# Kernel optimization log

Hardware: AMD Instinct MI355X
Metric: run time of the kernel (lower is better)

## Reference

```python
import jax, jax.numpy as jnp
import numpy as np

NL, D, Di, N, R, K, V, NH = 24, 768, 1536, 16, 48, 4, 50280, 12
BATCH, SEQ = 4, 256


def setup_inputs():
    key = jax.random.key(0)
    it = iter(jax.random.split(key, 48))
    g = lambda shape, s=0.02: jax.random.normal(next(it), shape, jnp.float32) * s
    inp = {
        "question_ids": jax.random.randint(next(it), (BATCH, SEQ), 0, V),
        "question_mask": jnp.ones((BATCH, SEQ), jnp.int32),
        "answer_ids": jax.random.randint(next(it), (BATCH, SEQ), 0, V),
        "answer_mask": jnp.ones((BATCH, SEQ), jnp.int32),
        "embed": g((V, D)),
        "norm_w": jnp.ones((NL, D)),
        "in_proj_w": g((NL, 2 * Di, D)),
        "conv_w": g((NL, Di, K), 0.1),
        "conv_b": jnp.zeros((NL, Di)),
        "x_proj_w": g((NL, R + 2 * N, Di)),
        "dt_proj_w": g((NL, Di, R)),
        "dt_proj_b": g((NL, Di), 0.5) - 4.0,
        "A_log": jnp.log(jnp.broadcast_to(jnp.arange(1, N + 1, dtype=jnp.float32), (NL, Di, N))) + 0.0,
        "D_p": jnp.ones((NL, Di)),
        "out_proj_w": g((NL, D, Di)),
        "norm_f": jnp.ones((D,)),
        "ln1_w": jnp.ones((D,)), "ln1_b": jnp.zeros((D,)),
        "qkv_w": g((3 * D, D)), "qkv_b": jnp.zeros((3 * D,)),
        "attn_out_w": g((D, D)), "attn_out_b": jnp.zeros((D,)),
        "ln2_w": jnp.ones((D,)), "ln2_b": jnp.zeros((D,)),
        "ff1_w": g((4 * D, D)), "ff1_b": jnp.zeros((4 * D,)),
        "ff2_w": g((D, 4 * D)), "ff2_b": jnp.zeros((D,)),
        "C_w": g((1, N)), "proj_out_w": g((D, Di)),
        "B_w": g((N, 1)), "proj_in_w": g((Di, D), 0.002),
    }
    return inp


def _rms(x, w, eps=1e-5):
    return x * jax.lax.rsqrt(jnp.mean(x * x, axis=-1, keepdims=True) + eps) * w


def _ln(x, w, b, eps=1e-5):
    m = jnp.mean(x, axis=-1, keepdims=True)
    v = jnp.var(x, axis=-1, keepdims=True)
    return (x - m) * jax.lax.rsqrt(v + eps) * w + b


def _mamba_block(h, layer, init_state):
    nw, ipw, cw, cb, xpw, dpw, dpb, alog, dp, opw = layer
    x_in = _rms(h, nw)
    xz = jnp.einsum('bld,ed->ble', x_in, ipw)  # (B,L,2*Di)
    x, z = jnp.split(xz, 2, axis=-1)
    L = x.shape[1]
    xp = jnp.pad(x, ((0, 0), (K - 1, 0), (0, 0)))  # causal depthwise conv, kernel K
    x = sum(xp[:, k:k + L, :] * cw[:, k] for k in range(K)) + cb
    x = jax.nn.silu(x)
    dbl = jnp.einsum('bld,ed->ble', x, xpw)
    dt, Bm, Cm = dbl[..., :R], dbl[..., R:R + N], dbl[..., R + N:]
    delta = jax.nn.softplus(jnp.einsum('blr,dr->bld', dt, dpw) + dpb)  # (B,L,Di)
    A = -jnp.exp(alog)  # (Di,N)

    def step(hs, t):  # selective scan, carry (B,Di,N)
        d_t, x_t, B_t, C_t = t
        hs = jnp.exp(d_t[..., None] * A) * hs + (d_t * x_t)[..., None] * B_t[:, None, :]
        return hs, jnp.einsum('bdn,bn->bd', hs, C_t)

    xs = tuple(jnp.moveaxis(a, 1, 0) for a in (delta, x, Bm, Cm))
    last, ys = jax.lax.scan(step, init_state, xs)
    y = jnp.moveaxis(ys, 0, 1) + x * dp
    y = y * jax.nn.silu(z)
    return h + jnp.einsum('bld,od->blo', y, opw), last


def _backbone(ids, mask, embed, mamba_params, norm_f, init_states):
    h = embed[ids] * mask[..., None].astype(embed.dtype)
    block = jax.checkpoint(_mamba_block)  # remat per layer: bounds bwd memory

    def layer_step(carry, xs):
        *layer, st = xs
        return block(carry, tuple(layer), st)

    h, lasts = jax.lax.scan(layer_step, h, mamba_params + (init_states,))
    h = _rms(h, norm_f)
    return jnp.einsum('bld,vd->blv', h, embed), lasts  # tied lm head


def _tf_layer(x, ln1_w, ln1_b, qkv_w, qkv_b, attn_out_w, attn_out_b, ln2_w, ln2_b, ff1_w, ff1_b, ff2_w, ff2_b):
    B, S, _ = x.shape
    hd = D // NH
    y = _ln(x, ln1_w, ln1_b)  # norm_first pre-LN
    q, k, v = jnp.split(y @ qkv_w.T + qkv_b, 3, axis=-1)
    q = q.reshape(B, S, NH, hd); k = k.reshape(B, S, NH, hd); v = v.reshape(B, S, NH, hd)
    att = jax.nn.softmax(jnp.einsum('bqhd,bkhd->bhqk', q, k) / jnp.sqrt(jnp.float32(hd)), axis=-1)
    o = jnp.einsum('bhqk,bkhd->bqhd', att, v).reshape(B, S, D)
    x = x + o @ attn_out_w.T + attn_out_b
    y = _ln(x, ln2_w, ln2_b)
    return x + jax.nn.gelu(y @ ff1_w.T + ff1_b, approximate=False) @ ff2_w.T + ff2_b


def _refine(states, C_w, proj_out_w, B_w, proj_in_w, tf_params):
    # states: (B, NL, Di, N); 12-step recurrent state refinement
    for _ in range(12):
        d = jnp.einsum('bsdn,n->bsd', states, C_w[0])  # C: Linear(16,1), squeeze(-1)
        d = jnp.einsum('bsd,od->bso', d, proj_out_w)   # 1536 -> 768
        d = _tf_layer(d, *tf_params)
        d = jnp.einsum('bso,do->bsd', d, proj_in_w)    # 768 -> 1536
        states = states + d[..., None] * B_w[:, 0]     # B: Linear(1,16)
    return states


def reference(question_ids, question_mask, answer_ids, answer_mask, embed, norm_w, in_proj_w, conv_w, conv_b, x_proj_w, dt_proj_w, dt_proj_b, A_log, D_p, out_proj_w, norm_f, ln1_w, ln1_b, qkv_w, qkv_b, attn_out_w, attn_out_b, ln2_w, ln2_b, ff1_w, ff1_b, ff2_w, ff2_b, C_w, proj_out_w, B_w, proj_in_w):
    mamba_params = (norm_w, in_proj_w, conv_w, conv_b, x_proj_w, dt_proj_w, dt_proj_b, A_log, D_p, out_proj_w)
    tf_params = (ln1_w, ln1_b, qkv_w, qkv_b, attn_out_w, attn_out_b, ln2_w, ln2_b, ff1_w, ff1_b, ff2_w, ff2_b)
    Bsz = question_ids.shape[0]
    zeros = jnp.zeros((NL, Bsz, Di, N), embed.dtype)
    _, lasts = _backbone(question_ids, question_mask, embed, mamba_params, norm_f, zeros)
    states = jnp.moveaxis(lasts, 0, 1)  # torch.stack(states, dim=1): (B, NL, Di, N)
    states = _refine(states, C_w, proj_out_w, B_w, proj_in_w, tf_params)
    logits, _ = _backbone(answer_ids, answer_mask, embed, mamba_params, norm_f, jnp.moveaxis(states, 0, 1))
    return logits
```

## Files before the change

### kernel.cpp

```cpp
#include <hip/hip_runtime.h>
#include <math.h>

namespace {

constexpr int kNL = 24, kD = 768, kDi = 1536, kN = 16, kR = 48, kK = 4, kV = 50280, kNH = 12;
constexpr int kB = 4, kS = 256;
constexpr int kMtok = kB * kS;
constexpr int kMref = kB * kNL;
constexpr int kVp = 50304;

using bf16x8   = __attribute__((ext_vector_type(8))) short;
using f32x4    = __attribute__((ext_vector_type(4))) float;
using ushort8v = __attribute__((ext_vector_type(8))) unsigned short;

__device__ __forceinline__ float siluf(float x) { return x / (1.f + __expf(-x)); }

__device__ __forceinline__ ushort f2b(float f) {
    union { float f; unsigned u; } v; v.f = f;
    unsigned u = v.u;
    unsigned r = (u + 0x7FFFu + ((u >> 16) & 1u)) >> 16;
    return (ushort)r;
}
__device__ __forceinline__ float b2f(ushort u) {
    union { unsigned u; float f; } v; v.u = (unsigned)u << 16; return v.f;
}

#define GLOAD_LDS(g, l) \
    __builtin_amdgcn_global_load_lds((const __attribute__((address_space(1))) void*)(g), \
                                     (__attribute__((address_space(3))) void*)(l), 16, 0, 0)

template <int BM, int BN, int BIAS, int ACT, int RES, int OUTMODE, int PIPE, int SSQ = 0>
__global__ __launch_bounds__(256, (PIPE == 3 ? 3 : 2)) void gemm_bf16(
    const ushort* __restrict__ A, int lda,
    const ushort* __restrict__ B, int ldb,
    float* __restrict__ C, int ldc,
    ushort* __restrict__ Cbf, int ldcb,
    float* __restrict__ C2,
    const float* __restrict__ bias,
    const float* __restrict__ aux,
    int M, int N, int K)
{
    constexpr int ACH = BM / 32;
    constexpr int BCH = BN / 32;
    constexpr int MI  = BM / 32;
    constexpr int NJ  = BN / 32;

    __shared__ ushort As[PIPE][BM * 64];
    __shared__ ushort Bs[PIPE][BN * 64];

    const int tid  = threadIdx.x;
    const int lane = tid & 63;
    const int wave = tid >> 6;
    const int m0 = blockIdx.y * BM;
    const int n0 = blockIdx.x * BN;
    const int wr = (wave >> 1) * (BM / 2);
    const int wc = (wave & 1) * (BN / 2);

    f32x4 acc[MI][NJ];
#pragma unroll
    for (int i = 0; i < MI; ++i)
#pragma unroll
        for (int j = 0; j < NJ; ++j) acc[i][j] = f32x4{0.f, 0.f, 0.f, 0.f};

    const int srow = lane >> 3;
    const int scol = ((lane & 7) ^ srow) * 8;
    const ushort* gA[ACH];
    const ushort* gB[BCH];
#pragma unroll
    for (int g = 0; g < ACH; ++g)
        gA[g] = A + (size_t)(m0 + (g * 4 + wave) * 8 + srow) * lda + scol;
#pragma unroll
    for (int g = 0; g < BCH; ++g)
        gB[g] = B + (size_t)(n0 + (g * 4 + wave) * 8 + srow) * ldb + scol;

    const int frow = lane & 15;
    const int kh   = lane >> 4;
    const int nt   = K >> 6;

    auto stage = [&](int t, int buf) {
        const int off = t * 64;
#pragma unroll
        for (int g = 0; g < ACH; ++g) GLOAD_LDS(gA[g] + off, &As[buf][(g * 4 + wave) * 512]);
#pragma unroll
        for (int g = 0; g < BCH; ++g) GLOAD_LDS(gB[g] + off, &Bs[buf][(g * 4 + wave) * 512]);
    };
    auto compute = [&](int buf) {
#pragma unroll
        for (int s = 0; s < 2; ++s) {
            bf16x8 fa[MI], fb[NJ];
#pragma unroll
            for (int i = 0; i < MI; ++i) {
                int r = wr + i * 16 + frow;
                int slot = (s * 4 + kh) ^ (r & 7);
                fa[i] = *(const bf16x8*)&As[buf][r * 64 + slot * 8];
            }
#pragma unroll
            for (int j = 0; j < NJ; ++j) {
                int r = wc + j * 16 + frow;
                int slot = (s * 4 + kh) ^ (r & 7);
                fb[j] = *(const bf16x8*)&Bs[buf][r * 64 + slot * 8];
            }
#pragma unroll
            for (int i = 0; i < MI; ++i)
#pragma unroll
                for (int j = 0; j < NJ; ++j)
                    acc[i][j] = __builtin_amdgcn_mfma_f32_16x16x32_bf16(fa[i], fb[j], acc[i][j], 0, 0, 0);
        }
    };

    if constexpr (PIPE == 3) {
        stage(0, 0);
        if (nt > 1) stage(1, 1);
        for (int t = 0; t < nt; ++t) {
            if (t < nt - 1) {
                asm volatile("s_waitcnt vmcnt(%0)" :: "n"(ACH + BCH) : "memory");
            } else {
                asm volatile("s_waitcnt vmcnt(0)" ::: "memory");
            }
            __builtin_amdgcn_s_barrier();
            if (t + 2 < nt) stage(t + 2, (t + 2) % 3);
            compute(t % 3);
        }
        __builtin_amdgcn_s_barrier();
    } else {
        stage(0, 0);
        __syncthreads();
        int cur = 0;
        for (int t = 0; t < nt; ++t) {
            if (t + 1 < nt) stage(t + 1, cur ^ 1);
            compute(cur);
            __syncthreads();
            cur ^= 1;
        }
    }

    const int ccol = lane & 15;
    const int crow = (lane >> 4) * 4;
    float rsq[MI][4];
    if constexpr (SSQ) {
#pragma unroll
        for (int i = 0; i < MI; ++i)
#pragma unroll
            for (int q = 0; q < 4; ++q) rsq[i][q] = 0.f;
    }
#pragma unroll
    for (int i = 0; i < MI; ++i) {
#pragma unroll
        for (int j = 0; j < NJ; ++j) {
            int gn = n0 + wc + j * 16 + ccol;
            if (gn >= N) continue;
            float bv = BIAS ? bias[gn] : 0.f;
#pragma unroll
            for (int q = 0; q < 4; ++q) {
                int gm = m0 + wr + i * 16 + crow + q;
                if (gm >= M) continue;
                float v = acc[i][j][q] + bv;
                if (ACT == 1) v = fmaxf(v, 0.f) + log1pf(expf(-fabsf(v)));
                if (ACT == 2) v = 0.5f * v * (1.f + erff(v * 0.70710678118654752f));
                if (OUTMODE == 3) {
                    if (gn < 48) Cbf[(size_t)gm * 64 + gn] = f2b(v);
                    else if (gn < 64) { Cbf[(size_t)gm * 64 + gn] = 0; C2[(size_t)(gn - 48) * kMtok + gm] = v; }
                    else if (gn < 80) C2[(size_t)(gn - 48) * kMtok + gm] = v;
                } else if (OUTMODE == 4) {
                    ((ushort*)C2)[(size_t)gn * kMtok + gm] = f2b(v);
                } else if (OUTMODE == 7) {
                    int bb = gm / kNL, ss = gm - bb * kNL;
                    float* stp = C2 + ((size_t)(ss * kB + bb) * kDi + gn) * kN;
                    float a2 = 0.f;
#pragma unroll
                    for (int nn = 0; nn < kN; ++nn) {
                        float sv = stp[nn] + v * bias[nn];
                        stp[nn] = sv;
                        a2 += sv * aux[nn];
                    }
                    Cbf[(size_t)gm * ldcb + gn] = f2b(a2);
                } else {
                    size_t ci = (size_t)gm * ldc + gn;
                    if (RES) v += C[ci];
                    if (OUTMODE != 2) C[ci] = v;
                    if (OUTMODE == 1 || OUTMODE == 2) Cbf[(size_t)gm * ldcb + gn] = f2b(v);
                    if constexpr (SSQ) rsq[i][q] += v * v;
                }
            }
        }
    }
    if constexpr (SSQ) {
#pragma unroll
        for (int i = 0; i < MI; ++i)
#pragma unroll
            for (int q = 0; q < 4; ++q) {
                rsq[i][q] += __shfl_xor(rsq[i][q], 1, 16);
                rsq[i][q] += __shfl_xor(rsq[i][q], 2, 16);
                rsq[i][q] += __shfl_xor(rsq[i][q], 4, 16);
                rsq[i][q] += __shfl_xor(rsq[i][q], 8, 16);
            }
        float* red = (float*)&As[0][0];
        __syncthreads();
        if ((lane & 15) == 0) {
#pragma unroll
            for (int i = 0; i < MI; ++i)
#pragma unroll
                for (int q = 0; q < 4; ++q) {
                    int rl = (wave >> 1) * 32 + i * 16 + (lane >> 4) * 4 + q;
                    red[(wave & 1) * 64 + rl] = rsq[i][q];
                }
        }
        __syncthreads();
        if (tid < 64) C2[(size_t)blockIdx.x * kMtok + m0 + tid] = red[tid] + red[64 + tid];
    }
}

template <int BM, int BN, int BIAS, int ACT, int RES, int OUTMODE, int PIPE, int SSQ = 0>
static void gemm(const ushort* A, int lda, const ushort* B, int ldb,
                 float* C, int ldc, ushort* Cb, int ldcb, float* C2,
                 const float* bias, const float* aux, int M, int N, int K, hipStream_t s)
{
    dim3 g((N + BN - 1) / BN, (M + BM - 1) / BM);
    gemm_bf16<BM, BN, BIAS, ACT, RES, OUTMODE, PIPE, SSQ><<<g, dim3(256), 0, s>>>(
        A, lda, B, ldb, C, ldc, Cb, ldcb, C2, bias, aux, M, N, K);
}

__global__ __launch_bounds__(256, 4) void gemm_rms(
    const float* __restrict__ hbuf, const float* __restrict__ ssq,
    const float* __restrict__ nw,
    const ushort* __restrict__ B, int ldb,
    ushort* __restrict__ Xbf, ushort* __restrict__ zTb,
    int M, int N, int K)
{
    constexpr int MI = 2, NJ = 2, BCH = 2;
    __shared__ ushort As[2][64 * 64];
    __shared__ ushort Bs[2][64 * 64];
    const int tid  = threadIdx.x;
    const int lane = tid & 63;
    const int wave = tid >> 6;
    const int m0 = blockIdx.y * 64;
    const int n0 = blockIdx.x * 64;
    const int wr = (wave >> 1) * 32;
    const int wc = (wave & 1) * 32;

    f32x4 acc[MI][NJ];
#pragma unroll
    for (int i = 0; i < MI; ++i)
#pragma unroll
        for (int j = 0; j < NJ; ++j) acc[i][j] = f32x4{0.f, 0.f, 0.f, 0.f};

    const int srow = lane >> 3;
    const int scol = ((lane & 7) ^ srow) * 8;
    const ushort* gB[BCH];
#pragma unroll
    for (int g = 0; g < BCH; ++g)
        gB[g] = B + (size_t)(n0 + (g * 4 + wave) * 8 + srow) * ldb + scol;

    int arow[2];
    float rs[2];
#pragma unroll
    for (int g = 0; g < 2; ++g) {
        arow[g] = m0 + (g * 4 + wave) * 8 + srow;
        float s = 0.f;
#pragma unroll
        for (int c = 0; c < 12; ++c) s += ssq[c * kMtok + arow[g]];
        rs[g] = rsqrtf(s * (1.f / 768.f) + 1e-5f);
    }

    const int frow = lane & 15;
    const int kh   = lane >> 4;
    const int nt   = K >> 6;

    float4 av[2][2], wv[2];
    auto loadA = [&](int t) {
        int k = t * 64 + scol;
        wv[0] = *(const float4*)&nw[k];
        wv[1] = *(const float4*)&nw[k + 4];
#pragma unroll
        for (int g = 0; g < 2; ++g) {
            av[g][0] = *(const float4*)&hbuf[(size_t)arow[g] * K + k];
            av[g][1] = *(const float4*)&hbuf[(size_t)arow[g] * K + k + 4];
        }
    };
    auto writeA = [&](int buf) {
#pragma unroll
        for (int g = 0; g < 2; ++g) {
            ushort8v o;
            o[0] = f2b(av[g][0].x * rs[g] * wv[0].x);
            o[1] = f2b(av[g][0].y * rs[g] * wv[0].y);
            o[2] = f2b(av[g][0].z * rs[g] * wv[0].z);
            o[3] = f2b(av[g][0].w * rs[g] * wv[0].w);
            o[4] = f2b(av[g][1].x * rs[g] * wv[1].x);
            o[5] = f2b(av[g][1].y * rs[g] * wv[1].y);
            o[6] = f2b(av[g][1].z * rs[g] * wv[1].z);
            o[7] = f2b(av[g][1].w * rs[g] * wv[1].w);
            *(ushort8v*)&As[buf][(g * 4 + wave) * 512 + lane * 8] = o;
        }
    };
    auto stageB = [&](int t, int buf) {
#pragma unroll
        for (int g = 0; g < BCH; ++g) GLOAD_LDS(gB[g] + t * 64, &Bs[buf][(g * 4 + wave) * 512]);
    };
    auto compute = [&](int buf) {
#pragma unroll
        for (int s = 0; s < 2; ++s) {
            bf16x8 fa[MI], fb[NJ];
#pragma unroll
            for (int i = 0; i < MI; ++i) {
                int r = wr + i * 16 + frow;
                int slot = (s * 4 + kh) ^ (r & 7);
                fa[i] = *(const bf16x8*)&As[buf][r * 64 + slot * 8];
            }
#pragma unroll
            for (int j = 0; j < NJ; ++j) {
                int r = wc + j * 16 + frow;
                int slot = (s * 4 + kh) ^ (r & 7);
                fb[j] = *(const bf16x8*)&Bs[buf][r * 64 + slot * 8];
            }
#pragma unroll
            for (int i = 0; i < MI; ++i)
#pragma unroll
                for (int j = 0; j < NJ; ++j)
                    acc[i][j] = __builtin_amdgcn_mfma_f32_16x16x32_bf16(fa[i], fb[j], acc[i][j], 0, 0, 0);
        }
    };

    loadA(0);
    stageB(0, 0);
    writeA(0);
    __syncthreads();
    int cur = 0;
    for (int t = 0; t < nt; ++t) {
        if (t + 1 < nt) { loadA(t + 1); stageB(t + 1, cur ^ 1); }
        compute(cur);
        if (t + 1 < nt) writeA(cur ^ 1);
        __syncthreads();
        cur ^= 1;
    }

    const int ccol = lane & 15;
    const int crow = (lane >> 4) * 4;
#pragma unroll
    for (int i = 0; i < MI; ++i) {
#pragma unroll
        for (int j = 0; j < NJ; ++j) {
            int gn = n0 + wc + j * 16 + ccol;
#pragma unroll
            for (int q = 0; q < 4; ++q) {
                int gm = m0 + wr + i * 16 + crow + q;
                float v = acc[i][j][q];
                if (gn < kDi) Xbf[(size_t)gm * kDi + gn] = f2b(v);
                else zTb[(size_t)(gn - kDi) * kMtok + gm] = f2b(siluf(v));
            }
        }
    }
}

__global__ void cvt_kernel(const float* __restrict__ src, ushort* __restrict__ dst, int n) {
    int i = (blockIdx.x * 256 + threadIdx.x) * 4;
    if (i >= n) return;
    float4 v = *(const float4*)(src + i);
    ushort4 o; o.x = f2b(v.x); o.y = f2b(v.y); o.z = f2b(v.z); o.w = f2b(v.w);
    *(ushort4*)(dst + i) = o;
}

__global__ void cvt_xpw_kernel(const float* __restrict__ src, ushort* __restrict__ dst) {
    int i = (blockIdx.x * 256 + threadIdx.x) * 4;
    if (i >= 24 * 80 * 1536) return;
    int l = i / (80 * 1536), r = i - l * (80 * 1536);
    int row = r / 1536, col = r - row * 1536;
    float4 v = *(const float4*)(src + i);
    ushort4 o; o.x = f2b(v.x); o.y = f2b(v.y); o.z = f2b(v.z); o.w = f2b(v.w);
    *(ushort4*)(dst + ((size_t)(l * 128 + row)) * 1536 + col) = o;
}

__global__ void cvt_dpw_kernel(const float* __restrict__ src, ushort* __restrict__ dst) {
    int i = blockIdx.x * 256 + threadIdx.x;
    if (i >= 24 * 1536 * 64) return;
    int col = i & 63, row = i >> 6;
    dst[i] = (col < 48) ? f2b(src[(size_t)row * 48 + col]) : (ushort)0;
}

__global__ void embed_kernel(const int* __restrict__ ids, const int* __restrict__ msk,
                             const float* __restrict__ embed, float* __restrict__ h,
                             float* __restrict__ ssq)
{
    int i = blockIdx.x * 256 + threadIdx.x;
    int row = i / kD, col = i - row * kD;
    float v = embed[(size_t)ids[row] * kD + col] * (float)msk[row];
    h[i] = v;
    float s = v * v;
    s += __shfl_xor(s, 1);  s += __shfl_xor(s, 2);  s += __shfl_xor(s, 4);
    s += __shfl_xor(s, 8);  s += __shfl_xor(s, 16); s += __shfl_xor(s, 32);
    if ((threadIdx.x & 63) == 0) ssq[(col >> 6) * kMtok + row] = s;
}

__global__ __launch_bounds__(256) void rms_kernel(const float* __restrict__ x,
                                                  const float* __restrict__ w,
                                                  ushort* __restrict__ out)
{
    __shared__ float red[256];
    int row = blockIdx.x, tid = threadIdx.x;
    const float* xr = x + (size_t)row * kD;
    float s = 0.f;
    for (int j = tid; j < kD; j += 256) { float v = xr[j]; s += v * v; }
    red[tid] = s; __syncthreads();
    for (int o = 128; o > 0; o >>= 1) { if (tid < o) red[tid] += red[tid + o]; __syncthreads(); }
    float rs = rsqrtf(red[0] / (float)kD + 1e-5f);
    for (int j = tid; j < kD; j += 256) out[(size_t)row * kD + j] = f2b(xr[j] * rs * w[j]);
}

__global__ __launch_bounds__(256) void ln_kernel(const float* __restrict__ x,
                                                 const float* __restrict__ w,
                                                 const float* __restrict__ b,
                                                 ushort* __restrict__ out)
{
    __shared__ float r1[256], r2[256];
    int row = blockIdx.x, tid = threadIdx.x;
    const float* xr = x + (size_t)row * kD;
    float s = 0.f, s2 = 0.f;
    for (int j = tid; j < kD; j += 256) { float v = xr[j]; s += v; s2 += v * v; }
    r1[tid] = s; r2[tid] = s2; __syncthreads();
    for (int o = 128; o > 0; o >>= 1) {
        if (tid < o) { r1[tid] += r1[tid + o]; r2[tid] += r2[tid + o]; }
        __syncthreads();
    }
    float mean = r1[0] / (float)kD;
    float var = r2[0] / (float)kD - mean * mean;
    float rsv = rsqrtf(var + 1e-5f);
    for (int j = tid; j < kD; j += 256)
        out[(size_t)row * kD + j] = f2b((xr[j] - mean) * rsv * w[j] + b[j]);
}

__global__ __launch_bounds__(256) void conv_kernel(
    const ushort* __restrict__ xb, const float* __restrict__ cw,
    const float* __restrict__ cb, ushort* __restrict__ xc_bf,
    ushort* __restrict__ xcT)
{
    int d   = blockIdx.x * 256 + threadIdx.x;
    int bt0 = blockIdx.y * 16;
    int t0  = bt0 & (kS - 1);
    float w0 = cw[d * 4], w1 = cw[d * 4 + 1], w2 = cw[d * 4 + 2], w3 = cw[d * 4 + 3];
    float bias = cb[d];
    float xv[19];
#pragma unroll
    for (int j = 0; j < 19; ++j) {
        int tt = t0 - 3 + j;
        xv[j] = (tt >= 0) ? b2f(xb[(size_t)(bt0 - 3 + j) * kDi + d]) : 0.f;
    }
    ushort8v o0, o1;
#pragma unroll
    for (int e = 0; e < 16; ++e) {
        float s = bias + xv[e] * w0 + xv[e + 1] * w1 + xv[e + 2] * w2 + xv[e + 3] * w3;
        ushort us = f2b(siluf(s));
        xc_bf[(size_t)(bt0 + e) * kDi + d] = us;
        if (e < 8) o0[e] = us; else o1[e - 8] = us;
    }
    *(ushort8v*)(xcT + (size_t)d * kMtok + bt0)     = o0;
    *(ushort8v*)(xcT + (size_t)d * kMtok + bt0 + 8) = o1;
}

__global__ __launch_bounds__(256) void scan_kernel(
    const ushort* __restrict__ dltT, const ushort* __restrict__ xcT,
    const ushort* __restrict__ zT, const float* __restrict__ bcT,
    const float* __restrict__ alog, const float* __restrict__ dp,
    float* __restrict__ states, ushort* __restrict__ y)
{
    int gid = blockIdx.x * 256 + threadIdx.x;
    int n = gid & 15;
    int d = (gid >> 4) % kDi;
    int b = gid / (kDi * kN);
    float Areg = -__expf(alog[d * kN + n]);
    float dpv = dp[d];
    size_t sidx = (size_t)(b * kDi + d) * kN + n;
    float hs = states[sidx];
    const ushort8v* pD = (const ushort8v*)(dltT + (size_t)d * kMtok + b * kS);
    const ushort8v* pX = (const ushort8v*)(xcT  + (size_t)d * kMtok + b * kS);
    const ushort8v* pZ = (const ushort8v*)(zT   + (size_t)d * kMtok + b * kS);
    const float4* pB = (const float4*)(bcT + (size_t)n * kMtok + b * kS);
    const float4* pC = (const float4*)(bcT + (size_t)(16 + n) * kMtok + b * kS);
    ushort8v D = pD[0], X = pX[0], Z = pZ[0];
    float4 B0 = pB[0], B1 = pB[1], C0 = pC[0], C1 = pC[1];
    ushort* yrow = y + (size_t)(b * kS) * kDi + d;
    for (int g = 0; g < kS / 8; ++g) {
        ushort8v Dn, Xn, Zn; float4 Bn0, Bn1, Cn0, Cn1;
        if (g + 1 < kS / 8) {
            Dn = pD[g + 1]; Xn = pX[g + 1]; Zn = pZ[g + 1];
            Bn0 = pB[2 * g + 2]; Bn1 = pB[2 * g + 3];
            Cn0 = pC[2 * g + 2]; Cn1 = pC[2 * g + 3];
        }
#pragma unroll
        for (int e = 0; e < 8; ++e) {
            float dv = b2f(D[e]), xv = b2f(X[e]), zv = b2f(Z[e]);
            float Bv = (e < 4) ? (&B0.x)[e] : (&B1.x)[e - 4];
            float Cv = (e < 4) ? (&C0.x)[e] : (&C1.x)[e - 4];
            hs = __expf(dv * Areg) * hs + (dv * xv) * Bv;
            float p = hs * Cv;
            p += __shfl_xor(p, 1, 16);
            p += __shfl_xor(p, 2, 16);
            p += __shfl_xor(p, 4, 16);
            p += __shfl_xor(p, 8, 16);
            if (n == 0) yrow[(size_t)(g * 8 + e) * kDi] = f2b((p + xv * dpv) * zv);
        }
        D = Dn; X = Xn; Z = Zn; B0 = Bn0; B1 = Bn1; C0 = Cn0; C1 = Cn1;
    }
    states[sidx] = hs;
}

__global__ void contract_kernel(const float* __restrict__ st, const float* __restrict__ Cw,
                                ushort* __restrict__ dDi)
{
    int i = blockIdx.x * 256 + threadIdx.x;
    int row = i / kDi, di = i - row * kDi;
    int b = row / kNL, s = row - b * kNL;
    const float* sp = st + ((size_t)(s * kB + b) * kDi + di) * kN;
    float acc = 0.f;
#pragma unroll
    for (int nn = 0; nn < kN; ++nn) acc += sp[nn] * Cw[nn];
    dDi[i] = f2b(acc);
}

__global__ __launch_bounds__(32) void attn_kernel(const float* __restrict__ qkv,
                                                  ushort* __restrict__ o)
{
    int b = blockIdx.x / kNH;
    int hh = blockIdx.x - b * kNH;
    int sq = threadIdx.x;
    if (sq >= kNL) return;
    const float* qrow = qkv + (size_t)(b * kNL + sq) * (3 * kD) + hh * 64;
    float q[64];
#pragma unroll
    for (int e = 0; e < 64; ++e) q[e] = qrow[e];
    float sc[kNL];
    float mx = -1e30f;
    for (int sk = 0; sk < kNL; ++sk) {
        const float* krow = qkv + (size_t)(b * kNL + sk) * (3 * kD) + kD + hh * 64;
        float dt = 0.f;
#pragma unroll
        for (int e = 0; e < 64; ++e) dt += q[e] * krow[e];
        dt *= 0.125f;
        sc[sk] = dt;
        mx = fmaxf(mx, dt);
    }
    float sum = 0.f;
    for (int sk = 0; sk < kNL; ++sk) { sc[sk] = expf(sc[sk] - mx); sum += sc[sk]; }
    float inv = 1.f / sum;
    float out[64];
#pragma unroll
    for (int e = 0; e < 64; ++e) out[e] = 0.f;
    for (int sk = 0; sk < kNL; ++sk) {
        float wgt = sc[sk] * inv;
        const float* vrow = qkv + (size_t)(b * kNL + sk) * (3 * kD) + 2 * kD + hh * 64;
#pragma unroll
        for (int e = 0; e < 64; ++e) out[e] += wgt * vrow[e];
    }
    ushort* orow = o + (size_t)(b * kNL + sq) * kD + hh * 64;
#pragma unroll
    for (int e = 0; e < 64; ++e) orow[e] = f2b(out[e]);
}

}

extern "C" void kernel_launch(void* const* d_in, const int* in_sizes, int n_in,
                              void* d_out, int out_size, void* d_ws, size_t ws_size,
                              hipStream_t stream)
{
    const int*   q_ids  = (const int*)d_in[0];
    const int*   q_msk  = (const int*)d_in[1];
    const int*   a_ids  = (const int*)d_in[2];
    const int*   a_msk  = (const int*)d_in[3];
    const float* embed  = (const float*)d_in[4];
    const float* norm_w = (const float*)d_in[5];
    const float* ipw    = (const float*)d_in[6];
    const float* cw     = (const float*)d_in[7];
    const float* cb     = (const float*)d_in[8];
    const float* xpw    = (const float*)d_in[9];
    const float* dpw    = (const float*)d_in[10];
    const float* dpb    = (const float*)d_in[11];
    const float* alog   = (const float*)d_in[12];
    const float* dpp    = (const float*)d_in[13];
    const float* opw    = (const float*)d_in[14];
    const float* norm_f = (const float*)d_in[15];
    const float* ln1w   = (const float*)d_in[16];
    const float* ln1b   = (const float*)d_in[17];
    const float* qkvw   = (const float*)d_in[18];
    const float* qkvbi  = (const float*)d_in[19];
    const float* aow    = (const float*)d_in[20];
    const float* aob    = (const float*)d_in[21];
    const float* ln2w   = (const float*)d_in[22];
    const float* ln2b   = (const float*)d_in[23];
    const float* ff1w   = (const float*)d_in[24];
    const float* ff1b   = (const float*)d_in[25];
    const float* ff2w   = (const float*)d_in[26];
    const float* ff2b   = (const float*)d_in[27];
    const float* Cwp    = (const float*)d_in[28];
    const float* powp   = (const float*)d_in[29];
    const float* Bwp    = (const float*)d_in[30];
    const float* piwp   = (const float*)d_in[31];

    char* base = (char*)d_ws;
    size_t cur = 0;
    auto allocB = [&](size_t bytes) { char* p = base + cur; cur = (cur + bytes + 255) & ~(size_t)255; return p; };
    auto allocF = [&](size_t n) { return (float*)allocB(n * 4); };
    auto allocH = [&](size_t n) { return (ushort*)allocB(n * 2); };

    float* h     = allocF((size_t)kMtok * kD);
    float* ssqp  = allocF((size_t)12 * kMtok);
    float* bcT   = allocF((size_t)32 * kMtok);
    float* st    = allocF((size_t)kNL * kB * kDi * kN);
    float* x768  = allocF((size_t)kMref * kD);
    float* qkvB  = allocF((size_t)kMref * 3 * kD);
    ushort* x_bf    = allocH((size_t)kMtok * kDi);
    ushort* zT_b    = allocH((size_t)kDi * kMtok);
    ushort* xcT_b   = allocH((size_t)kDi * kMtok);
    ushort* dltT_b  = allocH((size_t)kDi * kMtok);
    ushort* xc_bf   = allocH((size_t)kMtok * kDi);
    ushort* dtin_bf = allocH((size_t)kMtok * 64);
    ushort* yb_bf   = allocH((size_t)kMtok * kDi);
    ushort* xin_bf  = allocH((size_t)kMtok * kD);
    ushort* dDi_bf  = allocH((size_t)128 * kDi);
    ushort* tb_bf   = allocH((size_t)128 * kD);
    ushort* o768_bf = allocH((size_t)128 * kD);
    ushort* f3_bf   = allocH((size_t)128 * 4 * kD);
    ushort* x768_bf = allocH((size_t)128 * kD);
    ushort* xpw_bf  = allocH((size_t)kNL * 128 * kDi);
    ushort* dpw_bf  = allocH((size_t)kNL * kDi * 64);
    ushort* powp_bf = allocH((size_t)kD * kDi);
    ushort* qkvw_bf = allocH((size_t)3 * kD * kD);
    ushort* aow_bf  = allocH((size_t)kD * kD);
    ushort* ff1w_bf = allocH((size_t)4 * kD * kD);
    ushort* ff2w_bf = allocH((size_t)kD * 4 * kD);
    ushort* piw_bf  = allocH((size_t)kDi * kD);
    ushort* emb_bf  = allocH((size_t)kVp * kD);

    size_t base_end = cur;
    ushort* ipw_all = allocH((size_t)kNL * 2 * kDi * kD);
    ushort* opw_all = allocH((size_t)kNL * kD * kDi);
    bool full = (cur <= ws_size);
    ushort* ipw_stg = nullptr;
    ushort* opw_stg = nullptr;
    if (!full) {
        cur = base_end;
        ipw_stg = allocH((size_t)2 * kDi * kD);
        opw_stg = allocH((size_t)kD * kDi);
        if (cur > ws_size) return;
    }

    auto cvt = [&](const float* s, ushort* d, size_t n) {
        cvt_kernel<<<dim3((unsigned)((n / 4 + 255) / 256)), dim3(256), 0, stream>>>(s, d, (int)n);
    };

    hipMemsetAsync(st, 0, sizeof(float) * (size_t)kNL * kB * kDi * kN, stream);

    cvt_xpw_kernel<<<dim3(2880), dim3(256), 0, stream>>>(xpw, xpw_bf);
    cvt_dpw_kernel<<<dim3(9216), dim3(256), 0, stream>>>(dpw, dpw_bf);
    cvt(powp, powp_bf, (size_t)kD * kDi);
    cvt(qkvw, qkvw_bf, (size_t)3 * kD * kD);
    cvt(aow,  aow_bf,  (size_t)kD * kD);
    cvt(ff1w, ff1w_bf, (size_t)4 * kD * kD);
    cvt(ff2w, ff2w_bf, (size_t)kD * 4 * kD);
    cvt(piwp, piw_bf,  (size_t)kDi * kD);
    cvt(embed, emb_bf, (size_t)kV * kD);
    if (full) {
        cvt(ipw, ipw_all, (size_t)kNL * 2 * kDi * kD);
        cvt(opw, opw_all, (size_t)kNL * kD * kDi);
    }

    for (int pass = 0; pass < 2; ++pass) {
        const int* ids = pass ? a_ids : q_ids;
        const int* msk = pass ? a_msk : q_msk;

        embed_kernel<<<dim3(kMtok * kD / 256), dim3(256), 0, stream>>>(ids, msk, embed, h, ssqp);

        for (int l = 0; l < kNL; ++l) {
            const ushort* ipw_l;
            const ushort* opw_l;
            if (full) {
                ipw_l = ipw_all + (size_t)l * 2 * kDi * kD;
                opw_l = opw_all + (size_t)l * kD * kDi;
            } else {
                cvt(ipw + (size_t)l * 2 * kDi * kD, ipw_stg, (size_t)2 * kDi * kD);
                cvt(opw + (size_t)l * kD * kDi, opw_stg, (size_t)kD * kDi);
                ipw_l = ipw_stg;
                opw_l = opw_stg;
            }
            gemm_rms<<<dim3(48, 16), dim3(256), 0, stream>>>(
                h, ssqp, norm_w + (size_t)l * kD, ipw_l, kD, x_bf, zT_b, kMtok, 2 * kDi, kD);
            conv_kernel<<<dim3(kDi / 256, kMtok / 16), dim3(256), 0, stream>>>(
                x_bf, cw + (size_t)l * kDi * kK, cb + (size_t)l * kDi, xc_bf, xcT_b);
            gemm<64, 64, 0, 0, 0, 3, 3>(xc_bf, kDi, xpw_bf + (size_t)l * 128 * kDi, kDi,
                                        nullptr, 0, dtin_bf, 0, bcT,
                                        nullptr, nullptr, kMtok, 128, kDi, stream);
            gemm<64, 64, 1, 1, 0, 4, 3>(dtin_bf, 64, dpw_bf + (size_t)l * kDi * 64, 64,
                                        nullptr, 0, nullptr, 0, (float*)dltT_b,
                                        dpb + (size_t)l * kDi, nullptr, kMtok, kDi, 64, stream);
            scan_kernel<<<dim3(kB * kDi * kN / 256), dim3(256), 0, stream>>>(
                dltT_b, xcT_b, zT_b, bcT, alog + (size_t)l * kDi * kN, dpp + (size_t)l * kDi,
                st + (size_t)l * kB * kDi * kN, yb_bf);
            gemm<64, 64, 0, 0, 1, 0, 3, 1>(yb_bf, kDi, opw_l, kDi, h, kD, nullptr, 0, ssqp,
                                           nullptr, nullptr, kMtok, kD, kDi, stream);
        }

        if (pass == 0) {
            contract_kernel<<<dim3(kMref * kDi / 256), dim3(256), 0, stream>>>(st, Cwp, dDi_bf);
            for (int it = 0; it < 12; ++it) {
                gemm<64, 64, 0, 0, 0, 0, 3>(dDi_bf, kDi, powp_bf, kDi, x768, kD, nullptr, 0, nullptr,
                                            nullptr, nullptr, kMref, kD, kDi, stream);
                ln_kernel<<<dim3(kMref), dim3(256), 0, stream>>>(x768, ln1w, ln1b, tb_bf);
                gemm<64, 64, 1, 0, 0, 0, 3>(tb_bf, kD, qkvw_bf, kD, qkvB, 3 * kD, nullptr, 0, nullptr,
                                            qkvbi, nullptr, kMref, 3 * kD, kD, stream);
                attn_kernel<<<dim3(kB * kNH), dim3(32), 0, stream>>>(qkvB, o768_bf);
                gemm<64, 64, 1, 0, 1, 0, 3>(o768_bf, kD, aow_bf, kD, x768, kD, nullptr, 0, nullptr,
                                            aob, nullptr, kMref, kD, kD, stream);
                ln_kernel<<<dim3(kMref), dim3(256), 0, stream>>>(x768, ln2w, ln2b, tb_bf);
                gemm<64, 64, 1, 2, 0, 2, 3>(tb_bf, kD, ff1w_bf, kD, nullptr, 0, f3_bf, 4 * kD, nullptr,
                                            ff1b, nullptr, kMref, 4 * kD, kD, stream);
                gemm<64, 64, 1, 0, 1, 1, 3>(f3_bf, 4 * kD, ff2w_bf, 4 * kD, x768, kD, x768_bf, kD, nullptr,
                                            ff2b, nullptr, kMref, kD, 4 * kD, stream);
                gemm<64, 64, 0, 0, 0, 7, 3>(x768_bf, kD, piw_bf, kD, nullptr, 0, dDi_bf, kDi, st,
                                            Bwp, Cwp, kMref, kDi, kD, stream);
            }
        } else {
            rms_kernel<<<dim3(kMtok), dim3(256), 0, stream>>>(h, norm_f, xin_bf);
            gemm<128, 128, 0, 0, 0, 0, 2>(xin_bf, kD, emb_bf, kD, (float*)d_out, kV, nullptr, 0, nullptr,
                                          nullptr, nullptr, kMtok, kV, kD, stream);
        }
    }
}
```

Measured before the change: 8.637 ms.

## Fuse LayerNorm into GEMMs and fold ff2 with proj_in in refine loop

Removes the two standalone LayerNorm kernels in the refine loop. The preceding GEMMs now emit per-row partial sum and sum-of-squares, and a new gemm_ln kernel normalizes the A operand on the fly while staging it. It also precomputes proj_in·ff2 as one combined weight with a folded bias, so the ff2 GEMM and the proj_in GEMM become a single GEMM over a concatenated K=3840 operand [x | gelu(ff1)]. This cuts kernel launches and intermediate traffic in the 12-iteration refine loop, at the cost of extra setup GEMMs and different bf16 rounding from the reassociated products.

```diff
diff --git a/kernel.cpp b/kernel.cpp
--- a/kernel.cpp
+++ b/kernel.cpp
@@ -8,6 +8,7 @@
 constexpr int kMtok = kB * kS;
 constexpr int kMref = kB * kNL;
 constexpr int kVp = 50304;
+constexpr int kKa = 3840;
 
 using bf16x8   = __attribute__((ext_vector_type(8))) short;
 using f32x4    = __attribute__((ext_vector_type(4))) float;
@@ -38,6 +39,7 @@
     float* __restrict__ C2,
     const float* __restrict__ bias,
     const float* __restrict__ aux,
+    const float* __restrict__ aux2,
     int M, int N, int K)
 {
     constexpr int ACH = BM / 32;
@@ -136,12 +138,12 @@
 
     const int ccol = lane & 15;
     const int crow = (lane >> 4) * 4;
-    float rsq[MI][4];
+    float rsq[MI][4], rsm[MI][4];
     if constexpr (SSQ) {
 #pragma unroll
         for (int i = 0; i < MI; ++i)
 #pragma unroll
-            for (int q = 0; q < 4; ++q) rsq[i][q] = 0.f;
+            for (int q = 0; q < 4; ++q) { rsq[i][q] = 0.f; rsm[i][q] = 0.f; }
     }
 #pragma unroll
     for (int i = 0; i < MI; ++i) {
@@ -169,7 +171,7 @@
                     float a2 = 0.f;
 #pragma unroll
                     for (int nn = 0; nn < kN; ++nn) {
-                        float sv = stp[nn] + v * bias[nn];
+                        float sv = stp[nn] + v * aux2[nn];
                         stp[nn] = sv;
                         a2 += sv * aux[nn];
                     }
@@ -179,7 +181,7 @@
                     if (RES) v += C[ci];
                     if (OUTMODE != 2) C[ci] = v;
                     if (OUTMODE == 1 || OUTMODE == 2) Cbf[(size_t)gm * ldcb + gn] = f2b(v);
-                    if constexpr (SSQ) rsq[i][q] += v * v;
+                    if constexpr (SSQ) { rsq[i][q] += v * v; rsm[i][q] += v; }
                 }
             }
         }
@@ -193,6 +195,12 @@
                 rsq[i][q] += __shfl_xor(rsq[i][q], 2, 16);
                 rsq[i][q] += __shfl_xor(rsq[i][q], 4, 16);
                 rsq[i][q] += __shfl_xor(rsq[i][q], 8, 16);
+                if (SSQ == 2) {
+                    rsm[i][q] += __shfl_xor(rsm[i][q], 1, 16);
+                    rsm[i][q] += __shfl_xor(rsm[i][q], 2, 16);
+                    rsm[i][q] += __shfl_xor(rsm[i][q], 4, 16);
+                    rsm[i][q] += __shfl_xor(rsm[i][q], 8, 16);
+                }
             }
         float* red = (float*)&As[0][0];
         __syncthreads();
@@ -201,23 +209,33 @@
             for (int i = 0; i < MI; ++i)
 #pragma unroll
                 for (int q = 0; q < 4; ++q) {
-                    int rl = (wave >> 1) * 32 + i * 16 + (lane >> 4) * 4 + q;
-                    red[(wave & 1) * 64 + rl] = rsq[i][q];
+                    int rl = (wave >> 1) * (BM / 2) + i * 16 + (lane >> 4) * 4 + q;
+                    red[(wave & 1) * BM + rl] = rsq[i][q];
+                    if (SSQ == 2) red[2 * BM + (wave & 1) * BM + rl] = rsm[i][q];
                 }
         }
         __syncthreads();
-        if (tid < 64) C2[(size_t)blockIdx.x * kMtok + m0 + tid] = red[tid] + red[64 + tid];
+        if (tid < BM) {
+            if (SSQ == 1) {
+                C2[(size_t)blockIdx.x * kMtok + m0 + tid] = red[tid] + red[BM + tid];
+            } else {
+                C2[(size_t)blockIdx.x * 128 + m0 + tid] = red[tid] + red[BM + tid];
+                C2[(size_t)gridDim.x * 128 + blockIdx.x * 128 + m0 + tid] =
+                    red[2 * BM + tid] + red[3 * BM + tid];
+            }
+        }
     }
 }
 
 template <int BM, int BN, int BIAS, int ACT, int RES, int OUTMODE, int PIPE, int SSQ = 0>
 static void gemm(const ushort* A, int lda, const ushort* B, int ldb,
                  float* C, int ldc, ushort* Cb, int ldcb, float* C2,
-                 const float* bias, const float* aux, int M, int N, int K, hipStream_t s)
+                 const float* bias, const float* aux, int M, int N, int K, hipStream_t s,
+                 const float* aux2 = nullptr)
 {
     dim3 g((N + BN - 1) / BN, (M + BM - 1) / BM);
     gemm_bf16<BM, BN, BIAS, ACT, RES, OUTMODE, PIPE, SSQ><<<g, dim3(256), 0, s>>>(
-        A, lda, B, ldb, C, ldc, Cb, ldcb, C2, bias, aux, M, N, K);
+        A, lda, B, ldb, C, ldc, Cb, ldcb, C2, bias, aux, aux2, M, N, K);
 }
 
 __global__ __launch_bounds__(256, 4) void gemm_rms(
@@ -351,6 +369,151 @@
     }
 }
 
+template <int ACT, int OUTBF>
+__global__ __launch_bounds__(256, 4) void gemm_ln(
+    const float* __restrict__ hbuf, const float* __restrict__ pp,
+    const float* __restrict__ lw, const float* __restrict__ lb,
+    const ushort* __restrict__ B, int ldb,
+    float* __restrict__ C, int ldc,
+    ushort* __restrict__ Cbf, int ldcb,
+    const float* __restrict__ bias,
+    int M, int N, int K)
+{
+    constexpr int MI = 2, NJ = 2, BCH = 2, NP = 12;
+    __shared__ ushort As[2][64 * 64];
+    __shared__ ushort Bs[2][64 * 64];
+    const int tid  = threadIdx.x;
+    const int lane = tid & 63;
+    const int wave = tid >> 6;
+    const int m0 = blockIdx.y * 64;
+    const int n0 = blockIdx.x * 64;
+    const int wr = (wave >> 1) * 32;
+    const int wc = (wave & 1) * 32;
+
+    f32x4 acc[MI][NJ];
+#pragma unroll
+    for (int i = 0; i < MI; ++i)
+#pragma unroll
+        for (int j = 0; j < NJ; ++j) acc[i][j] = f32x4{0.f, 0.f, 0.f, 0.f};
+
+    const int srow = lane >> 3;
+    const int scol = ((lane & 7) ^ srow) * 8;
+    const ushort* gB[BCH];
+#pragma unroll
+    for (int g = 0; g < BCH; ++g)
+        gB[g] = B + (size_t)(n0 + (g * 4 + wave) * 8 + srow) * ldb + scol;
+
+    int arow[2];
+    float mean[2], rsv[2];
+#pragma unroll
+    for (int g = 0; g < 2; ++g) {
+        arow[g] = m0 + (g * 4 + wave) * 8 + srow;
+        float sq = 0.f, sm = 0.f;
+#pragma unroll
+        for (int c = 0; c < NP; ++c) {
+            sq += pp[c * 128 + arow[g]];
+            sm += pp[NP * 128 + c * 128 + arow[g]];
+        }
+        float mu = sm * (1.f / 768.f);
+        mean[g] = mu;
+        rsv[g] = rsqrtf(sq * (1.f / 768.f) - mu * mu + 1e-5f);
+    }
+
+    const int frow = lane & 15;
+    const int kh   = lane >> 4;
+    const int nt   = K >> 6;
+
+    float4 av[2][2], wv[2], bv2[2];
+    auto loadA = [&](int t) {
+        int k = t * 64 + scol;
+        wv[0]  = *(const float4*)&lw[k];
+        wv[1]  = *(const float4*)&lw[k + 4];
+        bv2[0] = *(const float4*)&lb[k];
+        bv2[1] = *(const float4*)&lb[k + 4];
+#pragma unroll
+        for (int g = 0; g < 2; ++g) {
+            av[g][0] = *(const float4*)&hbuf[(size_t)arow[g] * K + k];
+            av[g][1] = *(const float4*)&hbuf[(size_t)arow[g] * K + k + 4];
+        }
+    };
+    auto writeA = [&](int buf) {
+#pragma unroll
+        for (int g = 0; g < 2; ++g) {
+            ushort8v o;
+            o[0] = f2b((av[g][0].x - mean[g]) * rsv[g] * wv[0].x + bv2[0].x);
+            o[1] = f2b((av[g][0].y - mean[g]) * rsv[g] * wv[0].y + bv2[0].y);
+            o[2] = f2b((av[g][0].z - mean[g]) * rsv[g] * wv[0].z + bv2[0].z);
+            o[3] = f2b((av[g][0].w - mean[g]) * rsv[g] * wv[0].w + bv2[0].w);
+            o[4] = f2b((av[g][1].x - mean[g]) * rsv[g] * wv[1].x + bv2[1].x);
+            o[5] = f2b((av[g][1].y - mean[g]) * rsv[g] * wv[1].y + bv2[1].y);
+            o[6] = f2b((av[g][1].z - mean[g]) * rsv[g] * wv[1].z + bv2[1].z);
+            o[7] = f2b((av[g][1].w - mean[g]) * rsv[g] * wv[1].w + bv2[1].w);
+            *(ushort8v*)&As[buf][(g * 4 + wave) * 512 + lane * 8] = o;
+        }
+    };
+    auto stageB = [&](int t, int buf) {
+#pragma unroll
+        for (int g = 0; g < BCH; ++g) GLOAD_LDS(gB[g] + t * 64, &Bs[buf][(g * 4 + wave) * 512]);
+    };
+    auto compute = [&](int buf) {
+#pragma unroll
+        for (int s = 0; s < 2; ++s) {
+            bf16x8 fa[MI], fb[NJ];
+#pragma unroll
+            for (int i = 0; i < MI; ++i) {
+                int r = wr + i * 16 + frow;
+                int slot = (s * 4 + kh) ^ (r & 7);
+                fa[i] = *(const bf16x8*)&As[buf][r * 64 + slot * 8];
+            }
+#pragma unroll
+            for (int j = 0; j < NJ; ++j) {
+                int r = wc + j * 16 + frow;
+                int slot = (s * 4 + kh) ^ (r & 7);
+                fb[j] = *(const bf16x8*)&Bs[buf][r * 64 + slot * 8];
+            }
+#pragma unroll
+            for (int i = 0; i < MI; ++i)
+#pragma unroll
+                for (int j = 0; j < NJ; ++j)
+                    acc[i][j] = __builtin_amdgcn_mfma_f32_16x16x32_bf16(fa[i], fb[j], acc[i][j], 0, 0, 0);
+        }
+    };
+
+    loadA(0);
+    stageB(0, 0);
+    writeA(0);
+    __syncthreads();
+    int cur = 0;
+    for (int t = 0; t < nt; ++t) {
+        if (t + 1 < nt) { loadA(t + 1); stageB(t + 1, cur ^ 1); }
+        compute(cur);
+        if (t + 1 < nt) writeA(cur ^ 1);
+        __syncthreads();
+        cur ^= 1;
+    }
+
+    const int ccol = lane & 15;
+    const int crow = (lane >> 4) * 4;
+#pragma unroll
+    for (int i = 0; i < MI; ++i) {
+#pragma unroll
+        for (int j = 0; j < NJ; ++j) {
+            int gn = n0 + wc + j * 16 + ccol;
+            if (gn >= N) continue;
+            float bvv = bias[gn];
+#pragma unroll
+            for (int q = 0; q < 4; ++q) {
+                int gm = m0 + wr + i * 16 + crow + q;
+                if (gm >= M) continue;
+                float v = acc[i][j][q] + bvv;
+                if (ACT == 2) v = 0.5f * v * (1.f + erff(v * 0.70710678118654752f));
+                if (OUTBF) Cbf[(size_t)gm * ldcb + gn] = f2b(v);
+                else       C[(size_t)gm * ldc + gn] = v;
+            }
+        }
+    }
+}
+
 __global__ void cvt_kernel(const float* __restrict__ src, ushort* __restrict__ dst, int n) {
     int i = (blockIdx.x * 256 + threadIdx.x) * 4;
     if (i >= n) return;
@@ -374,6 +537,29 @@
     if (i >= 24 * 1536 * 64) return;
     int col = i & 63, row = i >> 6;
     dst[i] = (col < 48) ? f2b(src[(size_t)row * 48 + col]) : (ushort)0;
+}
+
+__global__ void cvt_ff2T_kernel(const float* __restrict__ src, ushort* __restrict__ dst) {
+    int i = blockIdx.x * 256 + threadIdx.x;
+    if (i >= 768 * 3072) return;
+    int d = i / 3072, f = i - d * 3072;
+    dst[(size_t)f * 768 + d] = f2b(src[i]);
+}
+
+__global__ void cvt_pi_kernel(const float* __restrict__ src, ushort* __restrict__ dst) {
+    int i = blockIdx.x * 256 + threadIdx.x;
+    if (i >= 1536 * 768) return;
+    int o = i / 768, d = i - o * 768;
+    dst[(size_t)o * kKa + d] = f2b(src[i]);
+}
+
+__global__ void pib_kernel(const float* __restrict__ piw, const float* __restrict__ ff2b,
+                           float* __restrict__ bias2) {
+    int o = blockIdx.x * 256 + threadIdx.x;
+    if (o >= 1536) return;
+    float s = 0.f;
+    for (int d = 0; d < 768; ++d) s += piw[(size_t)o * 768 + d] * ff2b[d];
+    bias2[o] = s;
 }
 
 __global__ void embed_kernel(const int* __restrict__ ids, const int* __restrict__ msk,
@@ -403,28 +589,6 @@
     for (int o = 128; o > 0; o >>= 1) { if (tid < o) red[tid] += red[tid + o]; __syncthreads(); }
     float rs = rsqrtf(red[0] / (float)kD + 1e-5f);
     for (int j = tid; j < kD; j += 256) out[(size_t)row * kD + j] = f2b(xr[j] * rs * w[j]);
-}
-
-__global__ __launch_bounds__(256) void ln_kernel(const float* __restrict__ x,
-                                                 const float* __restrict__ w,
-                                                 const float* __restrict__ b,
-                                                 ushort* __restrict__ out)
-{
-    __shared__ float r1[256], r2[256];
-    int row = blockIdx.x, tid = threadIdx.x;
-    const float* xr = x + (size_t)row * kD;
-    float s = 0.f, s2 = 0.f;
-    for (int j = tid; j < kD; j += 256) { float v = xr[j]; s += v; s2 += v * v; }
-    r1[tid] = s; r2[tid] = s2; __syncthreads();
-    for (int o = 128; o > 0; o >>= 1) {
-        if (tid < o) { r1[tid] += r1[tid + o]; r2[tid] += r2[tid + o]; }
-        __syncthreads();
-    }
-    float mean = r1[0] / (float)kD;
-    float var = r2[0] / (float)kD - mean * mean;
-    float rsv = rsqrtf(var + 1e-5f);
-    for (int j = tid; j < kD; j += 256)
-        out[(size_t)row * kD + j] = f2b((xr[j] - mean) * rsv * w[j] + b[j]);
 }
 
 __global__ __launch_bounds__(256) void conv_kernel(
@@ -603,8 +767,11 @@
     float* ssqp  = allocF((size_t)12 * kMtok);
     float* bcT   = allocF((size_t)32 * kMtok);
     float* st    = allocF((size_t)kNL * kB * kDi * kN);
-    float* x768  = allocF((size_t)kMref * kD);
-    float* qkvB  = allocF((size_t)kMref * 3 * kD);
+    float* x768  = allocF((size_t)128 * kD);
+    float* qkvB  = allocF((size_t)128 * 3 * kD);
+    float* bias2 = allocF((size_t)kDi);
+    float* pp1   = allocF((size_t)2 * 12 * 128);
+    float* pp2   = allocF((size_t)2 * 12 * 128);
     ushort* x_bf    = allocH((size_t)kMtok * kDi);
     ushort* zT_b    = allocH((size_t)kDi * kMtok);
     ushort* xcT_b   = allocH((size_t)kDi * kMtok);
@@ -614,18 +781,17 @@
     ushort* yb_bf   = allocH((size_t)kMtok * kDi);
     ushort* xin_bf  = allocH((size_t)kMtok * kD);
     ushort* dDi_bf  = allocH((size_t)128 * kDi);
-    ushort* tb_bf   = allocH((size_t)128 * kD);
     ushort* o768_bf = allocH((size_t)128 * kD);
-    ushort* f3_bf   = allocH((size_t)128 * 4 * kD);
-    ushort* x768_bf = allocH((size_t)128 * kD);
+    ushort* A2      = allocH((size_t)128 * kKa);
     ushort* xpw_bf  = allocH((size_t)kNL * 128 * kDi);
     ushort* dpw_bf  = allocH((size_t)kNL * kDi * 64);
     ushort* powp_bf = allocH((size_t)kD * kDi);
     ushort* qkvw_bf = allocH((size_t)3 * kD * kD);
     ushort* aow_bf  = allocH((size_t)kD * kD);
     ushort* ff1w_bf = allocH((size_t)4 * kD * kD);
-    ushort* ff2w_bf = allocH((size_t)kD * 4 * kD);
+    ushort* ff2wT   = allocH((size_t)4 * kD * kD);
     ushort* piw_bf  = allocH((size_t)kDi * kD);
+    ushort* B2      = allocH((size_t)kDi * kKa);
     ushort* emb_bf  = allocH((size_t)kVp * kD);
 
     size_t base_end = cur;
@@ -653,8 +819,12 @@
     cvt(qkvw, qkvw_bf, (size_t)3 * kD * kD);
     cvt(aow,  aow_bf,  (size_t)kD * kD);
     cvt(ff1w, ff1w_bf, (size_t)4 * kD * kD);
-    cvt(ff2w, ff2w_bf, (size_t)kD * 4 * kD);
     cvt(piwp, piw_bf,  (size_t)kDi * kD);
+    cvt_ff2T_kernel<<<dim3(9216), dim3(256), 0, stream>>>(ff2w, ff2wT);
+    cvt_pi_kernel<<<dim3(4608), dim3(256), 0, stream>>>(piwp, B2);
+    pib_kernel<<<dim3(6), dim3(256), 0, stream>>>(piwp, ff2b, bias2);
+    gemm<64, 64, 0, 0, 0, 2, 3>(piw_bf, kD, ff2wT, kD, nullptr, 0, B2 + kD, kKa, nullptr,
+                                nullptr, nullptr, kDi, 4 * kD, kD, stream);
     cvt(embed, emb_bf, (size_t)kV * kD);
     if (full) {
         cvt(ipw, ipw_all, (size_t)kNL * 2 * kDi * kD);
@@ -699,21 +869,19 @@
         if (pass == 0) {
             contract_kernel<<<dim3(kMref * kDi / 256), dim3(256), 0, stream>>>(st, Cwp, dDi_bf);
             for (int it = 0; it < 12; ++it) {
-                gemm<64, 64, 0, 0, 0, 0, 3>(dDi_bf, kDi, powp_bf, kDi, x768, kD, nullptr, 0, nullptr,
-                                            nullptr, nullptr, kMref, kD, kDi, stream);
-                ln_kernel<<<dim3(kMref), dim3(256), 0, stream>>>(x768, ln1w, ln1b, tb_bf);
-                gemm<64, 64, 1, 0, 0, 0, 3>(tb_bf, kD, qkvw_bf, kD, qkvB, 3 * kD, nullptr, 0, nullptr,
-                                            qkvbi, nullptr, kMref, 3 * kD, kD, stream);
+                gemm<64, 64, 0, 0, 0, 0, 3, 2>(dDi_bf, kDi, powp_bf, kDi, x768, kD, nullptr, 0, pp1,
+                                               nullptr, nullptr, kMref, kD, kDi, stream);
+                gemm_ln<0, 0><<<dim3(36, 2), dim3(256), 0, stream>>>(
+                    x768, pp1, ln1w, ln1b, qkvw_bf, kD, qkvB, 3 * kD, nullptr, 0, qkvbi,
+                    kMref, 3 * kD, kD);
                 attn_kernel<<<dim3(kB * kNH), dim3(32), 0, stream>>>(qkvB, o768_bf);
-                gemm<64, 64, 1, 0, 1, 0, 3>(o768_bf, kD, aow_bf, kD, x768, kD, nullptr, 0, nullptr,
-                                            aob, nullptr, kMref, kD, kD, stream);
-                ln_kernel<<<dim3(kMref), dim3(256), 0, stream>>>(x768, ln2w, ln2b, tb_bf);
-                gemm<64, 64, 1, 2, 0, 2, 3>(tb_bf, kD, ff1w_bf, kD, nullptr, 0, f3_bf, 4 * kD, nullptr,
-                                            ff1b, nullptr, kMref, 4 * kD, kD, stream);
-                gemm<64, 64, 1, 0, 1, 1, 3>(f3_bf, 4 * kD, ff2w_bf, 4 * kD, x768, kD, x768_bf, kD, nullptr,
-                                            ff2b, nullptr, kMref, kD, 4 * kD, stream);
-                gemm<64, 64, 0, 0, 0, 7, 3>(x768_bf, kD, piw_bf, kD, nullptr, 0, dDi_bf, kDi, st,
-                                            Bwp, Cwp, kMref, kDi, kD, stream);
+                gemm<64, 64, 1, 0, 1, 1, 3, 2>(o768_bf, kD, aow_bf, kD, x768, kD, A2, kKa, pp2,
+                                               aob, nullptr, kMref, kD, kD, stream);
+                gemm_ln<2, 1><<<dim3(48, 2), dim3(256), 0, stream>>>(
+                    x768, pp2, ln2w, ln2b, ff1w_bf, kD, nullptr, 0, A2 + kD, kKa, ff1b,
+                    kMref, 4 * kD, kD);
+                gemm<64, 64, 1, 0, 0, 7, 3>(A2, kKa, B2, kKa, nullptr, 0, dDi_bf, kDi, st,
+                                            bias2, Cwp, kMref, kDi, kKa, stream, Bwp);
             }
         } else {
             rms_kernel<<<dim3(kMtok), dim3(256), 0, stream>>>(h, norm_f, xin_bf);
```

Result: no change. 8.727 ms (+1.1%).
